# Performance work log

Hardware: AMD Instinct MI355X
Metric: run time of the kernel (lower is better)

Reference implementation:

```python
import jax, jax.numpy as jnp
import numpy as np

N = 100000      # nodes
E = 1600000     # edges (avg degree 16)
D_IN = 128
D_OUT = 128
P = 0.5         # dropout prob (module is in training mode)


def setup_inputs() -> dict:
    key = jax.random.key(0)
    k1, k2, k3 = jax.random.split(key, 3)
    x = jax.random.normal(k1, (N, D_IN), dtype=jnp.float32)
    edge_index = jax.random.randint(k2, (2, E), 0, N, dtype=jnp.int32)
    # GCNConv learned params (glorot-ish weight, zero bias)
    weight = jax.random.normal(k3, (D_IN, D_OUT), dtype=jnp.float32) / np.float32(np.sqrt(D_IN))
    bias = jnp.zeros((D_OUT,), dtype=jnp.float32)
    return {"x": x, "edge_index": edge_index, "weight": weight, "bias": bias}


def reference(x, edge_index, weight, bias):
    # --- GCNConv: add self-loops, symmetric deg^-1/2 normalization ---
    loops = jnp.arange(N, dtype=edge_index.dtype)
    src = jnp.concatenate([edge_index[0], loops])   # [E+N]
    dst = jnp.concatenate([edge_index[1], loops])   # [E+N]
    deg = jax.ops.segment_sum(jnp.ones_like(dst, dtype=x.dtype), dst, num_segments=N)
    dinv = jnp.where(deg > 0, jax.lax.rsqrt(deg), 0.0)          # deg^-1/2
    norm = dinv[src] * dinv[dst]                                # [E+N]
    h = x @ weight                                              # [N, D_OUT]
    msgs = h[src] * norm[:, None]                               # gather + scale
    out = jax.ops.segment_sum(msgs, dst, num_segments=N) + bias # scatter-add
    # --- ReLU ---
    out = jax.nn.relu(out)
    # --- Dropout (training=True), fixed key for determinism ---
    keep = jax.random.bernoulli(jax.random.key(42), 1.0 - P, out.shape)
    return jnp.where(keep, out / (1.0 - P), jnp.zeros((), out.dtype))
```

## Files before the change

### kernel.cpp

```cpp
#include <hip/hip_runtime.h>

#define N_NODES 100000
#define E_EDGES 1600000
#define D 128
#define PAD 136
#define GEMM_BLKS 1563
#define SCHUNK 4096
#define SCAT_BLKS ((E_EDGES + SCHUNK - 1) / SCHUNK)
#define RANGE 98
#define NR 1024
#define RCAP 2048
#define CAP 2048
#define NPW 13

typedef __attribute__((ext_vector_type(8))) short short8;
typedef __attribute__((ext_vector_type(8))) unsigned short ushort8v;
typedef __attribute__((ext_vector_type(4))) float f32x4;

__device__ __forceinline__ unsigned int rotl32(unsigned int x, int r) {
  return (x << r) | (x >> (32 - r));
}

__device__ __forceinline__ unsigned int threefry_bits(unsigned int ctr) {
  const unsigned int ks0 = 0u, ks1 = 42u;
  const unsigned int ks2 = ks0 ^ ks1 ^ 0x1BD11BDAu;
  unsigned int x0 = ks0;
  unsigned int x1 = ctr + ks1;
#define TF_ROUND(R) { x0 += x1; x1 = rotl32(x1, R); x1 ^= x0; }
  TF_ROUND(13) TF_ROUND(15) TF_ROUND(26) TF_ROUND(6)
  x0 += ks1; x1 += ks2 + 1u;
  TF_ROUND(17) TF_ROUND(29) TF_ROUND(16) TF_ROUND(24)
  x0 += ks2; x1 += ks0 + 2u;
  TF_ROUND(13) TF_ROUND(15) TF_ROUND(26) TF_ROUND(6)
  x0 += ks0; x1 += ks1 + 3u;
  TF_ROUND(17) TF_ROUND(29) TF_ROUND(16) TF_ROUND(24)
  x0 += ks1; x1 += ks2 + 4u;
  TF_ROUND(13) TF_ROUND(15) TF_ROUND(26) TF_ROUND(6)
  x0 += ks2; x1 += ks0 + 5u;
#undef TF_ROUND
  return x0 ^ x1;
}

__device__ __forceinline__ unsigned short f2bf(float f) {
  unsigned int u = __float_as_uint(f);
  u = (u + 0x7FFFu + ((u >> 16) & 1u)) >> 16;
  return (unsigned short)u;
}
__device__ __forceinline__ float bf2f_lo(unsigned int v) {
  return __uint_as_float(v << 16);
}
__device__ __forceinline__ float bf2f_hi(unsigned int v) {
  return __uint_as_float(v & 0xFFFF0000u);
}

__global__ __launch_bounds__(256) void k_init(const float* __restrict__ w,
                                              unsigned short* __restrict__ wbf,
                                              int* __restrict__ cur) {
  int t = blockIdx.x * 256 + threadIdx.x;
  int k = t >> 7;
  int n = t & 127;
  wbf[n * 128 + k] = f2bf(w[t]);
  if (t < NR) cur[t] = t * RCAP;
}

__global__ __launch_bounds__(256) void k_scat(const int* __restrict__ ei,
                                              int* __restrict__ cur,
                                              int* __restrict__ ebuf) {
  __shared__ int lcnt[NR];
  __shared__ int gb[NR];
  __shared__ int sc2[NR];
  const int t = threadIdx.x;
  const int e0 = blockIdx.x * SCHUNK;
  for (int i = t; i < NR; i += 256) { lcnt[i] = 0; sc2[i] = 0; }
  __syncthreads();
  int myd[SCHUNK / 256];
#pragma unroll
  for (int i = 0; i < SCHUNK / 256; ++i) {
    int e = e0 + i * 256 + t;
    myd[i] = -1;
    if (e < E_EDGES) {
      int d = ei[E_EDGES + e];
      myd[i] = d;
      atomicAdd(&lcnt[d / RANGE], 1);
    }
  }
  __syncthreads();
  for (int i = t; i < NR; i += 256) {
    int c = lcnt[i];
    gb[i] = c ? atomicAdd(&cur[i], c) : 0;
  }
  __syncthreads();
#pragma unroll
  for (int i = 0; i < SCHUNK / 256; ++i) {
    int d = myd[i];
    if (d >= 0) {
      int e = e0 + i * 256 + t;
      int s = ei[e];
      int b = d / RANGE;
      int dl = d - b * RANGE;
      int pos = gb[b] + atomicAdd(&sc2[b], 1);
      if (pos < (b + 1) * RCAP)
        ebuf[pos] = s | (dl << 17);
    }
  }
}

__global__ __launch_bounds__(256) void k_dg(const float* __restrict__ x,
                                            const unsigned short* __restrict__ wbf,
                                            unsigned short* __restrict__ h,
                                            const int* __restrict__ ebuf,
                                            const int* __restrict__ cur,
                                            float* __restrict__ dinv) {
  __shared__ unsigned short Wl[128 * PAD];
  __shared__ unsigned short Xl[64 * PAD];
  const int t = threadIdx.x;

  if (blockIdx.x < NR) {
    int* hist = (int*)Xl;
    const int r = blockIdx.x;
    if (t < 128) hist[t] = 0;
    __syncthreads();
    const int lo = r * RCAP;
    const int hi = min(cur[r], lo + RCAP);
    for (int e = lo + t; e < hi; e += 256)
      atomicAdd(&hist[((unsigned)ebuf[e]) >> 17], 1);
    __syncthreads();
    if (t < RANGE) {
      int n = r * RANGE + t;
      if (n < N_NODES) dinv[n] = rsqrtf((float)(hist[t] + 1));
    }
    return;
  }

  const int row0 = (blockIdx.x - NR) * 64;

#pragma unroll
  for (int i = 0; i < 8; ++i) {
    int u  = t + i * 256;
    int kg = u & 15;
    int n  = u >> 4;
    *(ushort8v*)&Wl[n * PAD + kg * 8] = *(const ushort8v*)&wbf[n * 128 + kg * 8];
  }
  const float4* x4 = (const float4*)x;
#pragma unroll
  for (int i = 0; i < 8; ++i) {
    int id = t + i * 256;
    int r  = id >> 5;
    int c4 = id & 31;
    int row = row0 + r; if (row >= N_NODES) row = N_NODES - 1;
    float4 v = x4[(long long)row * 32 + c4];
    ushort4 p;
    p.x = f2bf(v.x); p.y = f2bf(v.y); p.z = f2bf(v.z); p.w = f2bf(v.w);
    *(ushort4*)&Xl[r * PAD + c4 * 4] = p;
  }
  __syncthreads();

  const int wv   = t >> 6;
  const int l    = t & 63;
  const int quad = l >> 4;
  const int ln16 = l & 15;
  const int m0   = wv * 16;

  short8 a[4];
#pragma unroll
  for (int kt = 0; kt < 4; ++kt)
    a[kt] = *(const short8*)&Xl[(m0 + ln16) * PAD + kt * 32 + quad * 8];

#pragma unroll
  for (int nt = 0; nt < 8; ++nt) {
    f32x4 acc = {0.f, 0.f, 0.f, 0.f};
#pragma unroll
    for (int kt = 0; kt < 4; ++kt) {
      short8 b = *(const short8*)&Wl[(nt * 16 + ln16) * PAD + kt * 32 + quad * 8];
      acc = __builtin_amdgcn_mfma_f32_16x16x32_bf16(a[kt], b, acc, 0, 0, 0);
    }
#pragma unroll
    for (int r = 0; r < 4; ++r)
      Xl[(m0 + quad * 4 + r) * PAD + nt * 16 + ln16] = f2bf(acc[r]);
  }

#pragma unroll
  for (int v = 0; v < 4; ++v) {
    int idx = v * 64 + l;
    int rr  = idx >> 4;
    int ch  = idx & 15;
    int row = row0 + m0 + rr;
    if (row < N_NODES)
      *(ushort8v*)&h[(long long)row * D + ch * 8] = *(const ushort8v*)&Xl[(m0 + rr) * PAD + ch * 8];
  }
}

__global__ __launch_bounds__(512) void k_agg(const int* __restrict__ ebuf,
                                             const int* __restrict__ cur,
                                             const float* __restrict__ dinv,
                                             const unsigned short* __restrict__ h,
                                             const float* __restrict__ bias,
                                             float* __restrict__ out) {
  __shared__ int ssort[CAP];
  __shared__ int shist[128];
  __shared__ int sscn[128];
  __shared__ int scur[128];
  const int t  = threadIdx.x;
  const int r  = blockIdx.x;
  const int wv = t >> 6;
  const int l  = t & 63;
  const unsigned int* h32 = (const unsigned int*)h;

  float a0[NPW], a1[NPW];
#pragma unroll
  for (int j = 0; j < NPW; ++j) { a0[j] = 0.f; a1[j] = 0.f; }

  const int lo = r * RCAP;
  const int m  = min(cur[r], lo + RCAP) - lo;

  if (t < 128) shist[t] = 0;
  __syncthreads();

  int pk0 = -1, pk1 = -1, pk2 = -1, pk3 = -1;
  {
    int i0 = t, i1 = t + 512, i2 = t + 1024, i3 = t + 1536;
    if (i0 < m) { pk0 = ebuf[lo + i0]; atomicAdd(&shist[((unsigned)pk0) >> 17], 1); }
    if (i1 < m) { pk1 = ebuf[lo + i1]; atomicAdd(&shist[((unsigned)pk1) >> 17], 1); }
    if (i2 < m) { pk2 = ebuf[lo + i2]; atomicAdd(&shist[((unsigned)pk2) >> 17], 1); }
    if (i3 < m) { pk3 = ebuf[lo + i3]; atomicAdd(&shist[((unsigned)pk3) >> 17], 1); }
  }
  __syncthreads();

  if (t < 128) sscn[t] = shist[t];
  __syncthreads();
  for (int off = 1; off < 128; off <<= 1) {
    int xv = (t < 128 && t >= off) ? sscn[t - off] : 0;
    __syncthreads();
    if (t < 128) sscn[t] += xv;
    __syncthreads();
  }
  if (t < 128) scur[t] = sscn[t] - shist[t];
  __syncthreads();

  if (pk0 != -1) ssort[atomicAdd(&scur[((unsigned)pk0) >> 17], 1)] = pk0 & 0x1FFFF;
  if (pk1 != -1) ssort[atomicAdd(&scur[((unsigned)pk1) >> 17], 1)] = pk1 & 0x1FFFF;
  if (pk2 != -1) ssort[atomicAdd(&scur[((unsigned)pk2) >> 17], 1)] = pk2 & 0x1FFFF;
  if (pk3 != -1) ssort[atomicAdd(&scur[((unsigned)pk3) >> 17], 1)] = pk3 & 0x1FFFF;
  __syncthreads();

#pragma unroll
  for (int j = 0; j < NPW; ++j) {
    int nl = wv + 8 * j;
    if (nl < RANGE) {
      int s1i = sscn[nl];
      int s0i = s1i - shist[nl];
      float aa0 = a0[j], aa1 = a1[j];
#pragma unroll 4
      for (int e = s0i; e < s1i; ++e) {
        int s = ssort[e];
        float wgt = dinv[s];
        unsigned u = h32[(long long)s * 64 + l];
        aa0 = fmaf(bf2f_lo(u), wgt, aa0);
        aa1 = fmaf(bf2f_hi(u), wgt, aa1);
      }
      a0[j] = aa0; a1[j] = aa1;
    }
  }

#pragma unroll
  for (int j = 0; j < NPW; ++j) {
    int nl = wv + 8 * j;
    if (nl >= RANGE) continue;
    int n = r * RANGE + nl;
    if (n >= N_NODES) continue;
    float dv = rsqrtf((float)(shist[nl] + 1));
    unsigned hv = h32[(long long)n * 64 + l];
    float v0 = (a0[j] + bf2f_lo(hv) * dv) * dv;
    float v1 = (a1[j] + bf2f_hi(hv) * dv) * dv;
    float2 bb = ((const float2*)bias)[l];
    float r0 = fmaxf(v0 + bb.x, 0.f);
    float r1 = fmaxf(v1 + bb.y, 0.f);
    unsigned i0 = (unsigned)n * 128u + (unsigned)(2 * l);
    unsigned b0 = threefry_bits(i0);
    unsigned b1 = threefry_bits(i0 + 1u);
    float2 res;
    res.x = (b0 & 0x80000000u) ? 0.0f : r0 * 2.0f;
    res.y = (b1 & 0x80000000u) ? 0.0f : r1 * 2.0f;
    ((float2*)out)[(long long)n * 64 + l] = res;
  }
}

extern "C" void kernel_launch(void* const* d_in, const int* in_sizes, int n_in,
                              void* d_out, int out_size, void* d_ws, size_t ws_size,
                              hipStream_t stream) {
  const float* x    = (const float*)d_in[0];
  const int*   ei   = (const int*)d_in[1];
  const float* w    = (const float*)d_in[2];
  const float* bias = (const float*)d_in[3];
  float* out = (float*)d_out;

  char* p = (char*)d_ws;
  unsigned short* h   = (unsigned short*)p;  p += (size_t)N_NODES * D * 2;
  unsigned short* wbf = (unsigned short*)p;  p += 128 * 128 * 2;
  float* dinv = (float*)p;                   p += (size_t)(NR * RANGE) * 4;
  int* cur    = (int*)p;                     p += NR * 4;
  int* ebuf   = (int*)p;                     p += (size_t)NR * RCAP * 4;

  k_init<<<64, 256, 0, stream>>>(w, wbf, cur);
  k_scat<<<SCAT_BLKS, 256, 0, stream>>>(ei, cur, ebuf);
  k_dg<<<NR + GEMM_BLKS, 256, 0, stream>>>(x, wbf, h, ebuf, cur, dinv);
  k_agg<<<NR, 512, 0, stream>>>(ebuf, cur, dinv, h, bias, out);
}
```

Measured before the change: 218.4 us.

## Reuse histogram atomic ranks in scatter and prefetch dinv weights into shared memory

In the edge bucketing kernel, the rank returned by the first shared-memory atomic histogram pass is stored per edge and reused as the write offset. This drops the second atomic counter array and its atomics, and the chunk and block size are doubled. In the aggregation kernel, each edge's dinv[src] is loaded once during the bucket load and stored alongside the source index as an int2 in shared memory, which removes the dependent global dinv load from the inner gather loop. The cost is doubled LDS use for the sorted edge array (16 KB) and more registers per scatter thread.

```diff
diff --git a/kernel.cpp b/kernel.cpp
--- a/kernel.cpp
+++ b/kernel.cpp
@@ -5,7 +5,7 @@
 #define D 128
 #define PAD 136
 #define GEMM_BLKS 1563
-#define SCHUNK 4096
+#define SCHUNK 8192
 #define SCAT_BLKS ((E_EDGES + SCHUNK - 1) / SCHUNK)
 #define RANGE 98
 #define NR 1024
@@ -63,42 +63,42 @@
   if (t < NR) cur[t] = t * RCAP;
 }
 
-__global__ __launch_bounds__(256) void k_scat(const int* __restrict__ ei,
+__global__ __launch_bounds__(512) void k_scat(const int* __restrict__ ei,
                                               int* __restrict__ cur,
                                               int* __restrict__ ebuf) {
   __shared__ int lcnt[NR];
   __shared__ int gb[NR];
-  __shared__ int sc2[NR];
   const int t = threadIdx.x;
   const int e0 = blockIdx.x * SCHUNK;
-  for (int i = t; i < NR; i += 256) { lcnt[i] = 0; sc2[i] = 0; }
-  __syncthreads();
-  int myd[SCHUNK / 256];
-#pragma unroll
-  for (int i = 0; i < SCHUNK / 256; ++i) {
-    int e = e0 + i * 256 + t;
+  for (int i = t; i < NR; i += 512) lcnt[i] = 0;
+  __syncthreads();
+  int myd[SCHUNK / 512];
+  int myr[SCHUNK / 512];
+#pragma unroll
+  for (int i = 0; i < SCHUNK / 512; ++i) {
+    int e = e0 + i * 512 + t;
     myd[i] = -1;
     if (e < E_EDGES) {
       int d = ei[E_EDGES + e];
       myd[i] = d;
-      atomicAdd(&lcnt[d / RANGE], 1);
-    }
-  }
-  __syncthreads();
-  for (int i = t; i < NR; i += 256) {
+      myr[i] = atomicAdd(&lcnt[d / RANGE], 1);
+    }
+  }
+  __syncthreads();
+  for (int i = t; i < NR; i += 512) {
     int c = lcnt[i];
     gb[i] = c ? atomicAdd(&cur[i], c) : 0;
   }
   __syncthreads();
 #pragma unroll
-  for (int i = 0; i < SCHUNK / 256; ++i) {
+  for (int i = 0; i < SCHUNK / 512; ++i) {
     int d = myd[i];
     if (d >= 0) {
-      int e = e0 + i * 256 + t;
+      int e = e0 + i * 512 + t;
       int s = ei[e];
       int b = d / RANGE;
       int dl = d - b * RANGE;
-      int pos = gb[b] + atomicAdd(&sc2[b], 1);
+      int pos = gb[b] + myr[i];
       if (pos < (b + 1) * RCAP)
         ebuf[pos] = s | (dl << 17);
     }
@@ -196,7 +196,7 @@
                                              const unsigned short* __restrict__ h,
                                              const float* __restrict__ bias,
                                              float* __restrict__ out) {
-  __shared__ int ssort[CAP];
+  __shared__ int2 sswp[CAP];
   __shared__ int shist[128];
   __shared__ int sscn[128];
   __shared__ int scur[128];
@@ -217,12 +217,13 @@
   __syncthreads();
 
   int pk0 = -1, pk1 = -1, pk2 = -1, pk3 = -1;
+  float w0 = 0.f, w1 = 0.f, w2 = 0.f, w3 = 0.f;
   {
     int i0 = t, i1 = t + 512, i2 = t + 1024, i3 = t + 1536;
-    if (i0 < m) { pk0 = ebuf[lo + i0]; atomicAdd(&shist[((unsigned)pk0) >> 17], 1); }
-    if (i1 < m) { pk1 = ebuf[lo + i1]; atomicAdd(&shist[((unsigned)pk1) >> 17], 1); }
-    if (i2 < m) { pk2 = ebuf[lo + i2]; atomicAdd(&shist[((unsigned)pk2) >> 17], 1); }
-    if (i3 < m) { pk3 = ebuf[lo + i3]; atomicAdd(&shist[((unsigned)pk3) >> 17], 1); }
+    if (i0 < m) { pk0 = ebuf[lo + i0]; w0 = dinv[pk0 & 0x1FFFF]; atomicAdd(&shist[((unsigned)pk0) >> 17], 1); }
+    if (i1 < m) { pk1 = ebuf[lo + i1]; w1 = dinv[pk1 & 0x1FFFF]; atomicAdd(&shist[((unsigned)pk1) >> 17], 1); }
+    if (i2 < m) { pk2 = ebuf[lo + i2]; w2 = dinv[pk2 & 0x1FFFF]; atomicAdd(&shist[((unsigned)pk2) >> 17], 1); }
+    if (i3 < m) { pk3 = ebuf[lo + i3]; w3 = dinv[pk3 & 0x1FFFF]; atomicAdd(&shist[((unsigned)pk3) >> 17], 1); }
   }
   __syncthreads();
 
@@ -237,10 +238,10 @@
   if (t < 128) scur[t] = sscn[t] - shist[t];
   __syncthreads();
 
-  if (pk0 != -1) ssort[atomicAdd(&scur[((unsigned)pk0) >> 17], 1)] = pk0 & 0x1FFFF;
-  if (pk1 != -1) ssort[atomicAdd(&scur[((unsigned)pk1) >> 17], 1)] = pk1 & 0x1FFFF;
-  if (pk2 != -1) ssort[atomicAdd(&scur[((unsigned)pk2) >> 17], 1)] = pk2 & 0x1FFFF;
-  if (pk3 != -1) ssort[atomicAdd(&scur[((unsigned)pk3) >> 17], 1)] = pk3 & 0x1FFFF;
+  if (pk0 != -1) sswp[atomicAdd(&scur[((unsigned)pk0) >> 17], 1)] = make_int2(pk0 & 0x1FFFF, __float_as_int(w0));
+  if (pk1 != -1) sswp[atomicAdd(&scur[((unsigned)pk1) >> 17], 1)] = make_int2(pk1 & 0x1FFFF, __float_as_int(w1));
+  if (pk2 != -1) sswp[atomicAdd(&scur[((unsigned)pk2) >> 17], 1)] = make_int2(pk2 & 0x1FFFF, __float_as_int(w2));
+  if (pk3 != -1) sswp[atomicAdd(&scur[((unsigned)pk3) >> 17], 1)] = make_int2(pk3 & 0x1FFFF, __float_as_int(w3));
   __syncthreads();
 
 #pragma unroll
@@ -252,9 +253,9 @@
       float aa0 = a0[j], aa1 = a1[j];
 #pragma unroll 4
       for (int e = s0i; e < s1i; ++e) {
-        int s = ssort[e];
-        float wgt = dinv[s];
-        unsigned u = h32[(long long)s * 64 + l];
+        int2 p = sswp[e];
+        float wgt = __int_as_float(p.y);
+        unsigned u = h32[(long long)p.x * 64 + l];
         aa0 = fmaf(bf2f_lo(u), wgt, aa0);
         aa1 = fmaf(bf2f_hi(u), wgt, aa1);
       }
@@ -302,7 +303,7 @@
   int* ebuf   = (int*)p;                     p += (size_t)NR * RCAP * 4;
 
   k_init<<<64, 256, 0, stream>>>(w, wbf, cur);
-  k_scat<<<SCAT_BLKS, 256, 0, stream>>>(ei, cur, ebuf);
+  k_scat<<<SCAT_BLKS, 512, 0, stream>>>(ei, cur, ebuf);
   k_dg<<<NR + GEMM_BLKS, 256, 0, stream>>>(x, wbf, h, ebuf, cur, dinv);
   k_agg<<<NR, 512, 0, stream>>>(ebuf, cur, dinv, h, bias, out);
 }
```

Result: slower. 223.7 us (+2.5%).
